# Kernel optimization log

Measured on AMD Instinct MI355X. Metric: run time of the kernel, lower is better.

The kernel has to match this reference:

```python
import jax, jax.numpy as jnp
import numpy as np

POS_RATIO = 0.5
EPS = 1e-6


def setup_inputs() -> dict:
    key = jax.random.key(0)
    k1, k2, k3, k4 = jax.random.split(key, 4)
    N, C, D, H, W = 8, 256, 8, 16, 16
    q = jax.random.normal(k1, (N, C, D, H, W), dtype=jnp.float32)
    k = jax.random.normal(k2, (N, C, D, H, W), dtype=jnp.float32)
    # coords: (x0, y0, z0, x1, y1, z1) with lower-right > upper-left
    uq = jax.random.uniform(k3, (N, 3), dtype=jnp.float32) * 0.5
    uk = jax.random.uniform(k4, (N, 3), dtype=jnp.float32) * 0.5
    coord_q = jnp.concatenate([uq, uq + 0.5], axis=1)
    coord_k = jnp.concatenate([uk, uk + 0.5], axis=1)
    return {"q": q, "k": k, "coord_q": coord_q, "coord_k": coord_k}


def _centers(coord, D, H, W):
    """Per-batch voxel-center coordinates. coord: [N,6]. Returns cx, cy, cz each [N, D*H*W], plus bin diag [N]."""
    bw = (coord[:, 3] - coord[:, 0]) / W  # [N]
    bh = (coord[:, 4] - coord[:, 1]) / H
    bd = (coord[:, 5] - coord[:, 2]) / D
    gz, gy, gx = jnp.meshgrid(jnp.arange(D, dtype=coord.dtype),
                              jnp.arange(H, dtype=coord.dtype),
                              jnp.arange(W, dtype=coord.dtype), indexing="ij")
    gx = (gx + 0.5).reshape(-1)[None, :]  # [1, DHW]
    gy = (gy + 0.5).reshape(-1)[None, :]
    gz = (gz + 0.5).reshape(-1)[None, :]
    cx = gx * bw[:, None] + coord[:, 0][:, None]
    cy = gy * bh[:, None] + coord[:, 1][:, None]
    cz = gz * bd[:, None] + coord[:, 2][:, None]
    diag = jnp.sqrt(bw ** 2 + bh ** 2 + bd ** 2)  # [N]
    return cx, cy, cz, diag


def reference(q, k, coord_q, coord_k):
    N, C, D, H, W = q.shape
    qf = q.reshape(N, C, -1)  # [N, C, P], P = D*H*W
    kf = k.reshape(N, C, -1)
    cqx, cqy, cqz, q_diag = _centers(coord_q, D, H, W)
    ckx, cky, ckz, k_diag = _centers(coord_k, D, H, W)
    max_diag = jnp.maximum(q_diag, k_diag)  # [N]
    # pairwise center distance, normalized by max bin diagonal: [N, P, P]
    dist = jnp.sqrt((cqx[:, :, None] - ckx[:, None, :]) ** 2
                    + (cqy[:, :, None] - cky[:, None, :]) ** 2
                    + (cqz[:, :, None] - ckz[:, None, :]) ** 2) / max_diag[:, None, None]
    pos_mask = jax.lax.stop_gradient((dist < POS_RATIO).astype(q.dtype))
    # logit[n, p, p'] = sum_c q[n,c,p] * k[n,c,p']
    logit = jnp.einsum("ncp,ncq->npq", qf, kf)
    loss = (logit * pos_mask).sum((-2, -1)) / (pos_mask.sum((-2, -1)) + EPS)  # [N]
    return -2.0 * loss.mean()
```

## Files before the change

kernel.cpp:

```cpp
#include <hip/hip_runtime.h>
#include <cstdint>
#include <cstddef>

#define NB 8
#define CH 256
#define DD 8
#define HH 16
#define WW 16
#define PP 2048

#define OFF_DPART 16384

__device__ __forceinline__ int z_window(float czq, float bdk, float k2, float maxd) {
    float lim = 0.500060f * maxd;
    int zk0 = -1;
    #pragma unroll
    for (int zk = 0; zk < DD; ++zk) {
        float czk = __fadd_rn(__fmul_rn(__fadd_rn((float)zk, 0.5f), bdk), k2);
        bool feas = fabsf(__fsub_rn(czq, czk)) < lim;
        if (feas && zk0 < 0) zk0 = zk;
    }
    if (zk0 > DD - 2) zk0 = DD - 2;
    return zk0;
}

typedef __attribute__((address_space(3))) void       lds_void;
typedef __attribute__((address_space(1))) const void glb_void;

#define CC 16
__global__ __launch_bounds__(256) void fused_kernel(
    const float* __restrict__ q, const float* __restrict__ k,
    const float* __restrict__ coord_q, const float* __restrict__ coord_k,
    float* __restrict__ partial, float* __restrict__ dpart)
{
    __shared__ float klds[CC][512];

    int t  = threadIdx.x;
    int wv = t >> 6;
    int lane = t & 63;
    int cg = blockIdx.x;
    int zq = blockIdx.y;
    int n  = blockIdx.z;
    int flat = (n * 8 + zq) * 16 + cg;
    int c0 = cg * CC;

    const float* cq = coord_q + n * 6;
    const float* ck = coord_k + n * 6;
    float q0 = cq[0], q1 = cq[1], q2 = cq[2];
    float k0 = ck[0], k1 = ck[1], k2 = ck[2];
    float bwq = __fdiv_rn(__fsub_rn(cq[3], q0), (float)WW);
    float bhq = __fdiv_rn(__fsub_rn(cq[4], q1), (float)HH);
    float bdq = __fdiv_rn(__fsub_rn(cq[5], q2), (float)DD);
    float bwk = __fdiv_rn(__fsub_rn(ck[3], k0), (float)WW);
    float bhk = __fdiv_rn(__fsub_rn(ck[4], k1), (float)HH);
    float bdk = __fdiv_rn(__fsub_rn(ck[5], k2), (float)DD);
    float diagq = __fsqrt_rn(__fadd_rn(__fadd_rn(__fmul_rn(bwq, bwq), __fmul_rn(bhq, bhq)),
                                       __fmul_rn(bdq, bdq)));
    float diagk = __fsqrt_rn(__fadd_rn(__fadd_rn(__fmul_rn(bwk, bwk), __fmul_rn(bhk, bhk)),
                                       __fmul_rn(bdk, bdk)));
    float maxd = fmaxf(diagq, diagk);
    float cqz = __fadd_rn(__fmul_rn(__fadd_rn((float)zq, 0.5f), bdq), q2);

    int zk0 = z_window(cqz, bdk, k2, maxd);

    float acc = 0.0f;
    int cnt = 0;

    if (zk0 >= 0) {
        float lim = 0.500060f * maxd;

        float czk0 = __fadd_rn(__fmul_rn(__fadd_rn((float)zk0, 0.5f), bdk), k2);
        float czk1 = __fadd_rn(__fmul_rn(__fadd_rn((float)(zk0 + 1), 0.5f), bdk), k2);
        bool feas0 = fabsf(__fsub_rn(cqz, czk0)) < lim;
        bool feas1 = fabsf(__fsub_rn(cqz, czk1)) < lim;

        {
            int u = (t & 63) << 2;
            if (feas0) {
                const float* ksrc = k + ((size_t)(n * CH + c0)) * PP + (zk0 << 8);
                #pragma unroll
                for (int i = 0; i < 4; ++i) {
                    int c = i * 4 + wv;
                    const float* src = ksrc + (size_t)c * PP + u;
                    float* dst = &klds[c][u];
                    __builtin_amdgcn_global_load_lds((const glb_void*)src,
                                                     (lds_void*)dst, 16, 0, 0);
                }
            }
            if (feas1) {
                const float* ksrc = k + ((size_t)(n * CH + c0)) * PP + ((zk0 + 1) << 8);
                #pragma unroll
                for (int i = 0; i < 4; ++i) {
                    int c = i * 4 + wv;
                    const float* src = ksrc + (size_t)c * PP + u;
                    float* dst = &klds[c][256 + u];
                    __builtin_amdgcn_global_load_lds((const glb_void*)src,
                                                     (lds_void*)dst, 16, 0, 0);
                }
            }
        }

        int p = (zq << 8) + t;
        float qv[CC];
        {
            const float* qcol = q + ((size_t)(n * CH + c0)) * PP + p;
            #pragma unroll
            for (int c = 0; c < CC; ++c)
                qv[c] = qcol[(size_t)c * PP];
        }

        int ix = t & 15, iy = (t >> 4) & 15;
        float cqx = __fadd_rn(__fmul_rn(__fadd_rn((float)ix, 0.5f), bwq), q0);
        float cqy = __fadd_rn(__fmul_rn(__fadd_rn((float)iy, 0.5f), bhq), q1);

        float tx = (cqx - k0) / bwk - 0.5f;
        float ty = (cqy - k1) / bhk - 0.5f;
        float rx = lim / bwk + 0.03f;
        float ry = lim / bhk + 0.03f;
        int jx0 = (int)ceilf(tx - rx);  if (jx0 < 0) jx0 = 0;
        int jx1 = (int)floorf(tx + rx); if (jx1 > WW - 1) jx1 = WW - 1;
        int jy0 = (int)ceilf(ty - ry);  if (jy0 < 0) jy0 = 0;
        int jy1 = (int)floorf(ty + ry); if (jy1 > HH - 1) jy1 = HH - 1;

        float half_maxd = 0.5f * maxd;
        float thr2 = half_maxd * half_maxd * 1.001f;

        float s[CC];
        #pragma unroll
        for (int c = 0; c < CC; ++c) s[c] = 0.0f;

        __syncthreads();

        for (int dzI = 0; dzI < 2; ++dzI) {
            if (dzI == 0 ? !feas0 : !feas1) continue;
            int jz = zk0 + dzI;
            float ckz = __fadd_rn(__fmul_rn(__fadd_rn((float)jz, 0.5f), bdk), k2);
            float dz  = __fsub_rn(cqz, ckz);
            float dz2 = __fmul_rn(dz, dz);
            for (int jy = jy0; jy <= jy1; ++jy) {
                float cky = __fadd_rn(__fmul_rn(__fadd_rn((float)jy, 0.5f), bhk), k1);
                float dy  = __fsub_rn(cqy, cky);
                float dy2 = __fmul_rn(dy, dy);
                for (int jx = jx0; jx <= jx1; ++jx) {
                    float ckx = __fadd_rn(__fmul_rn(__fadd_rn((float)jx, 0.5f), bwk), k0);
                    float dx  = __fsub_rn(cqx, ckx);
                    float dx2 = __fmul_rn(dx, dx);
                    float d2  = __fadd_rn(__fadd_rn(dx2, dy2), dz2);
                    bool pos = false;
                    if (d2 < thr2) {
                        float dist = __fdiv_rn(__fsqrt_rn(d2), maxd);
                        pos = dist < 0.5f;
                    }
                    if (pos) {
                        ++cnt;
                        int idx = (dzI << 8) + (jy << 4) + jx;
                        #pragma unroll
                        for (int c = 0; c < CC; ++c)
                            s[c] += klds[c][idx];
                    }
                }
            }
        }

        #pragma unroll
        for (int c = 0; c < CC; ++c)
            acc += qv[c] * s[c];
    }

    int ci = cnt;
    #pragma unroll
    for (int off = 32; off > 0; off >>= 1) {
        acc += __shfl_down(acc, off, 64);
        ci  += __shfl_down(ci, off, 64);
    }
    if (lane == 0) {
        partial[flat * 4 + wv] = acc;
        if (cg == 0) dpart[(n * 8 + zq) * 4 + wv] = (float)ci;
    }
}

__global__ __launch_bounds__(512) void final_kernel(const float* __restrict__ partial,
                                                    const float* __restrict__ dpart,
                                                    float* __restrict__ out)
{
    __shared__ float numsh[NB];
    __shared__ float densh[NB];
    int t = threadIdx.x;
    int n = t >> 6, lane = t & 63;

    float sp = 0.0f;
    #pragma unroll
    for (int i = 0; i < 8; ++i)
        sp += partial[n * 512 + i * 64 + lane];
    float sc = (lane < 32) ? dpart[n * 32 + lane] : 0.0f;
    #pragma unroll
    for (int off = 32; off > 0; off >>= 1) {
        sp += __shfl_down(sp, off, 64);
        sc += __shfl_down(sc, off, 64);
    }
    if (lane == 0) { numsh[n] = sp; densh[n] = sc; }
    __syncthreads();
    if (t == 0) {
        float r = 0.0f;
        for (int i = 0; i < NB; ++i)
            r += numsh[i] / (densh[i] + 1e-6f);
        out[0] = -2.0f * (r / (float)NB);
    }
}

extern "C" void kernel_launch(void* const* d_in, const int* in_sizes, int n_in,
                              void* d_out, int out_size, void* d_ws, size_t ws_size,
                              hipStream_t stream) {
    const float* q       = (const float*)d_in[0];
    const float* k       = (const float*)d_in[1];
    const float* coord_q = (const float*)d_in[2];
    const float* coord_k = (const float*)d_in[3];
    float* out = (float*)d_out;

    char* w = (char*)d_ws;
    float* partial = (float*)w;
    float* dpart   = (float*)(w + OFF_DPART);

    fused_kernel<<<dim3(CH / CC, DD, NB), 256, 0, stream>>>(q, k, coord_q, coord_k,
                                                            partial, dpart);
    final_kernel<<<1, 512, 0, stream>>>(partial, dpart, out);
}
```

Before: 80.56 us.

## Transpose K tile to point-major LDS and gather via precomputed bitmask

K staging now goes through registers into an LDS tile transposed to [point][channel] instead of using direct global-to-LDS loads, so each neighbour's 16 channels come back as four float4 LDS reads. The distance tests run first and record positive neighbours in a 64-bit mask per z-slice. This overlaps the global load latency with the mask computation, and the accumulation loop then walks only the set bits. The risks are higher register pressure from the staging arrays, possible LDS bank conflicts on the strided float4 writes, and the assumption that the x/y window never spans more than 8 cells.

```diff
diff --git a/kernel.cpp b/kernel.cpp
--- a/kernel.cpp
+++ b/kernel.cpp
@@ -24,16 +24,13 @@
     return zk0;
 }
 
-typedef __attribute__((address_space(3))) void       lds_void;
-typedef __attribute__((address_space(1))) const void glb_void;
-
 #define CC 16
 __global__ __launch_bounds__(256) void fused_kernel(
     const float* __restrict__ q, const float* __restrict__ k,
     const float* __restrict__ coord_q, const float* __restrict__ coord_k,
     float* __restrict__ partial, float* __restrict__ dpart)
 {
-    __shared__ float klds[CC][512];
+    __shared__ __align__(16) float klds[512][CC];
 
     int t  = threadIdx.x;
     int wv = t >> 6;
@@ -74,30 +71,24 @@
         bool feas0 = fabsf(__fsub_rn(cqz, czk0)) < lim;
         bool feas1 = fabsf(__fsub_rn(cqz, czk1)) < lim;
 
-        {
-            int u = (t & 63) << 2;
-            if (feas0) {
-                const float* ksrc = k + ((size_t)(n * CH + c0)) * PP + (zk0 << 8);
+        int pr = t >> 2, cquad = t & 3;
+        const float* kbase = k + ((size_t)(n * CH + c0)) * PP;
+        float st0[16], st1[16];
+        if (feas0) {
+            const float* g = kbase + (zk0 << 8);
+            #pragma unroll
+            for (int i = 0; i < 4; ++i)
                 #pragma unroll
-                for (int i = 0; i < 4; ++i) {
-                    int c = i * 4 + wv;
-                    const float* src = ksrc + (size_t)c * PP + u;
-                    float* dst = &klds[c][u];
-                    __builtin_amdgcn_global_load_lds((const glb_void*)src,
-                                                     (lds_void*)dst, 16, 0, 0);
-                }
-            }
-            if (feas1) {
-                const float* ksrc = k + ((size_t)(n * CH + c0)) * PP + ((zk0 + 1) << 8);
+                for (int j = 0; j < 4; ++j)
+                    st0[i * 4 + j] = g[(size_t)(cquad * 4 + j) * PP + (i * 64 + pr)];
+        }
+        if (feas1) {
+            const float* g = kbase + ((zk0 + 1) << 8);
+            #pragma unroll
+            for (int i = 0; i < 4; ++i)
                 #pragma unroll
-                for (int i = 0; i < 4; ++i) {
-                    int c = i * 4 + wv;
-                    const float* src = ksrc + (size_t)c * PP + u;
-                    float* dst = &klds[c][256 + u];
-                    __builtin_amdgcn_global_load_lds((const glb_void*)src,
-                                                     (lds_void*)dst, 16, 0, 0);
-                }
-            }
+                for (int j = 0; j < 4; ++j)
+                    st1[i * 4 + j] = g[(size_t)(cquad * 4 + j) * PP + (i * 64 + pr)];
         }
 
         int p = (zq << 8) + t;
@@ -125,18 +116,14 @@
         float half_maxd = 0.5f * maxd;
         float thr2 = half_maxd * half_maxd * 1.001f;
 
-        float s[CC];
-        #pragma unroll
-        for (int c = 0; c < CC; ++c) s[c] = 0.0f;
-
-        __syncthreads();
-
+        unsigned long long m0 = 0ull, m1 = 0ull;
         for (int dzI = 0; dzI < 2; ++dzI) {
             if (dzI == 0 ? !feas0 : !feas1) continue;
             int jz = zk0 + dzI;
             float ckz = __fadd_rn(__fmul_rn(__fadd_rn((float)jz, 0.5f), bdk), k2);
-            float dz  = __fsub_rn(cqz, ckz);
-            float dz2 = __fmul_rn(dz, dz);
+            float dzf = __fsub_rn(cqz, ckz);
+            float dz2 = __fmul_rn(dzf, dzf);
+            unsigned long long mm = 0ull;
             for (int jy = jy0; jy <= jy1; ++jy) {
                 float cky = __fadd_rn(__fmul_rn(__fadd_rn((float)jy, 0.5f), bhk), k1);
                 float dy  = __fsub_rn(cqy, cky);
@@ -151,15 +138,57 @@
                         float dist = __fdiv_rn(__fsqrt_rn(d2), maxd);
                         pos = dist < 0.5f;
                     }
-                    if (pos) {
-                        ++cnt;
-                        int idx = (dzI << 8) + (jy << 4) + jx;
-                        #pragma unroll
-                        for (int c = 0; c < CC; ++c)
-                            s[c] += klds[c][idx];
-                    }
+                    if (pos)
+                        mm |= 1ull << (((jy - jy0) << 3) | (jx - jx0));
                 }
             }
+            if (dzI == 0) m0 = mm; else m1 = mm;
+        }
+
+        if (feas0) {
+            #pragma unroll
+            for (int i = 0; i < 4; ++i) {
+                float4 v = make_float4(st0[i*4+0], st0[i*4+1], st0[i*4+2], st0[i*4+3]);
+                *reinterpret_cast<float4*>(&klds[i * 64 + pr][cquad * 4]) = v;
+            }
+        }
+        if (feas1) {
+            #pragma unroll
+            for (int i = 0; i < 4; ++i) {
+                float4 v = make_float4(st1[i*4+0], st1[i*4+1], st1[i*4+2], st1[i*4+3]);
+                *reinterpret_cast<float4*>(&klds[256 + i * 64 + pr][cquad * 4]) = v;
+            }
+        }
+
+        float s[CC];
+        #pragma unroll
+        for (int c = 0; c < CC; ++c) s[c] = 0.0f;
+
+        __syncthreads();
+
+        while (m0) {
+            int slot = __builtin_ctzll(m0);
+            m0 &= m0 - 1;
+            int idx = ((jy0 + (slot >> 3)) << 4) + (jx0 + (slot & 7));
+            const float4* r = reinterpret_cast<const float4*>(&klds[idx][0]);
+            float4 v0 = r[0], v1 = r[1], v2 = r[2], v3 = r[3];
+            s[0]  += v0.x; s[1]  += v0.y; s[2]  += v0.z; s[3]  += v0.w;
+            s[4]  += v1.x; s[5]  += v1.y; s[6]  += v1.z; s[7]  += v1.w;
+            s[8]  += v2.x; s[9]  += v2.y; s[10] += v2.z; s[11] += v2.w;
+            s[12] += v3.x; s[13] += v3.y; s[14] += v3.z; s[15] += v3.w;
+            ++cnt;
+        }
+        while (m1) {
+            int slot = __builtin_ctzll(m1);
+            m1 &= m1 - 1;
+            int idx = 256 + (((jy0 + (slot >> 3)) << 4) + (jx0 + (slot & 7)));
+            const float4* r = reinterpret_cast<const float4*>(&klds[idx][0]);
+            float4 v0 = r[0], v1 = r[1], v2 = r[2], v3 = r[3];
+            s[0]  += v0.x; s[1]  += v0.y; s[2]  += v0.z; s[3]  += v0.w;
+            s[4]  += v1.x; s[5]  += v1.y; s[6]  += v1.z; s[7]  += v1.w;
+            s[8]  += v2.x; s[9]  += v2.y; s[10] += v2.z; s[11] += v2.w;
+            s[12] += v3.x; s[13] += v3.y; s[14] += v3.z; s[15] += v3.w;
+            ++cnt;
         }
 
         #pragma unroll
```

After: 80.12 us. No clear change (-0.5%).
